# Performance work log

Hardware: AMD Instinct MI355X
Metric: run time of the kernel (lower is better)

Reference implementation:

```python
import jax, jax.numpy as jnp
import numpy as np

B, T, F = 2048, 256, 128
H = F  # hidden_size == feature_num in lstm0


def setup_inputs() -> dict:
    key = jax.random.key(0)
    ks = jax.random.split(key, 7)
    s = 1.0 / np.sqrt(H)  # torch LSTM/Linear default uniform init scale
    s_lin = 1.0 / np.sqrt(T * H)
    return {
        "x": jax.random.normal(ks[0], (B, T, F), dtype=jnp.float32),
        "w_ih": jax.random.uniform(ks[1], (4 * H, F), jnp.float32, -s, s),
        "w_hh": jax.random.uniform(ks[2], (4 * H, H), jnp.float32, -s, s),
        "b_ih": jax.random.uniform(ks[3], (4 * H,), jnp.float32, -s, s),
        "b_hh": jax.random.uniform(ks[4], (4 * H,), jnp.float32, -s, s),
        "w_lin": jax.random.uniform(ks[5], (1, T * H), jnp.float32, -s_lin, s_lin),
        "b_lin": jax.random.uniform(ks[6], (1,), jnp.float32, -s_lin, s_lin),
    }


def _lstm(x, w_ih, w_hh, b_ih, b_hh):
    # x: [B, T, F] -> h_seq: [B, T, H]; torch gate order: i, f, g, o
    b = x.shape[0]
    h_dim = w_hh.shape[1]
    # precompute input contribution for all timesteps: [B, T, 4H]
    xg = jnp.einsum('btf,gf->btg', x, w_ih) + b_ih + b_hh

    def step(carry, g_t):  # g_t: [B, 4H]
        h, c = carry
        gates = g_t + h @ w_hh.T
        i, f, g, o = jnp.split(gates, 4, axis=-1)
        c = jax.nn.sigmoid(f) * c + jax.nn.sigmoid(i) * jnp.tanh(g)
        h = jax.nn.sigmoid(o) * jnp.tanh(c)
        return (h, c), h

    init = (jnp.zeros((b, h_dim), x.dtype), jnp.zeros((b, h_dim), x.dtype))
    _, hs = jax.lax.scan(step, init, jnp.swapaxes(xg, 0, 1))  # hs: [T, B, H]
    return jnp.swapaxes(hs, 0, 1)


def reference(x, w_ih, w_hh, b_ih, b_hh, w_lin, b_lin):
    h = _lstm(x, w_ih, w_hh, b_ih, b_hh)          # [B, T, H]
    # Dropout(0.6) in eval mode == identity
    flat = h.reshape(h.shape[0], -1)               # [B, T*H]
    out = flat @ w_lin.T + b_lin                   # [B, 1]
    return out.reshape(-1)                          # [B]
```

## Files before the change

kernel.cpp:

```cpp
#include <hip/hip_runtime.h>


typedef __attribute__((ext_vector_type(8))) short short8;
typedef __attribute__((ext_vector_type(4))) float f32x4;
typedef __attribute__((ext_vector_type(2))) float f32x2;

#define T_STEPS 256
#define L2E 1.4426950408889634f

__device__ __forceinline__ unsigned int cvt_pk_bf16(float lo, float hi) {
    unsigned int r;
    asm volatile("v_cvt_pk_bf16_f32 %0, %1, %2" : "=v"(r) : "v"(lo), "v"(hi));
    return r;
}
__device__ __forceinline__ unsigned short f2bf(float f) {
    unsigned int u = __builtin_bit_cast(unsigned int, f);
    u += 0x7fffu + ((u >> 16) & 1u);
    return (unsigned short)(u >> 16);
}
__device__ __forceinline__ float rcp_fast(float x) { return __builtin_amdgcn_rcpf(x); }
__device__ __forceinline__ float exp2f_fast(float x) { return __builtin_amdgcn_exp2f(x); }

__device__ __forceinline__ short8 pack8(const f32x4 a, const f32x4 b) {
    short8 v;
    v[0] = (short)f2bf(a[0]); v[1] = (short)f2bf(a[1]);
    v[2] = (short)f2bf(a[2]); v[3] = (short)f2bf(a[3]);
    v[4] = (short)f2bf(b[0]); v[5] = (short)f2bf(b[1]);
    v[6] = (short)f2bf(b[2]); v[7] = (short)f2bf(b[3]);
    return v;
}

#define LBAR() asm volatile("s_waitcnt lgkmcnt(0)\n\ts_barrier" ::: "memory")

#define MFMA16(A, B, C) __builtin_amdgcn_mfma_f32_16x16x32_bf16((A), (B), (C), 0, 0, 0)

#define GATE(R, CS, WL, AJ, HO)                                                \
  { float gi = ch0[0][R] + ch1[0][R];                                          \
    float gf = ch0[1][R] + ch1[1][R];                                          \
    float gg = ch0[2][R] + ch1[2][R];                                          \
    float go = ch0[3][R] + ch1[3][R];                                          \
    float ef = exp2f_fast(gf * L2E);                                           \
    float ei = exp2f_fast(gi * L2E);                                           \
    float eg = exp2f_fast(gg * (2.f * L2E));                                   \
    float Fq = ef + 1.f, Iq = ei + 1.f, Gq = eg + 1.f;                         \
    float pq = Iq * Gq;                                                        \
    float Rq = rcp_fast(Fq * pq);                                              \
    float cq = __builtin_fmaf(ef * pq, (CS), (ei * Fq) * (eg - 1.f)) * Rq;     \
    (CS) = cq;                                                                 \
    float ccq = fminf(fmaxf(cq, -15.f), 15.f);                                 \
    float eo = exp2f_fast(go * L2E);                                           \
    float ec = exp2f_fast(ccq * (2.f * L2E));                                  \
    float oh = (eo * (ec - 1.f)) * rcp_fast((eo + 1.f) * (ec + 1.f));          \
    (AJ) = __builtin_fmaf(oh, (WL), (AJ));                                     \
    (HO) = oh; }

#define GROUP(T0, GP, GXC, GXN)                                                \
  do {                                                                         \
    const f32x4 zero4 = {0.f, 0.f, 0.f, 0.f};                                  \
    short8 afh[4], afx0, afx1;                                                 \
    f32x4 ch0[4], ch1[4];                                                      \
                         \
    _Pragma("unroll")                                                          \
    for (int kt = 0; kt < 4; ++kt)                                             \
      afh[kt] = *reinterpret_cast<const short8*>(&hbuf[0][hridx[kt]]);         \
    __builtin_amdgcn_s_setprio(1);                                             \
    _Pragma("unroll")                                                          \
    for (int n = 0; n < 4; ++n) ch0[n] = MFMA16(afh[0], bq[4][n], GXC[n]);     \
    _Pragma("unroll")                                                          \
    for (int n = 0; n < 4; ++n) ch1[n] = MFMA16(afh[2], bq[6][n], zero4);      \
    _Pragma("unroll")                                                          \
    for (int n = 0; n < 4; ++n) ch0[n] = MFMA16(afh[1], bq[5][n], ch0[n]);     \
    _Pragma("unroll")                                                          \
    for (int n = 0; n < 4; ++n) ch1[n] = MFMA16(afh[3], bq[7][n], ch1[n]);     \
    __builtin_amdgcn_s_setprio(0);                                             \
          \
    afx0 = *reinterpret_cast<const short8*>(&xbuf[GP][xridx[0]]);              \
    afx1 = *reinterpret_cast<const short8*>(&xbuf[GP][xridx[1]]);              \
    _Pragma("unroll")                                                          \
    for (int n = 0; n < 4; ++n)                                                \
      GXN[n] = (f32x4){bias[n], bias[n], bias[n], bias[n]};                    \
    _Pragma("unroll")                                                          \
    for (int n = 0; n < 4; ++n) GXN[n] = MFMA16(afx0, bq[0][n], GXN[n]);       \
    _Pragma("unroll")                                                          \
    for (int n = 0; n < 4; ++n) GXN[n] = MFMA16(afx1, bq[1][n], GXN[n]);       \
    {                      \
      const int tt = ((T0) + 4 < T_STEPS) ? (T0) + 4 : 0;                      \
      nx0 = *reinterpret_cast<const f32x2*>(xrow + (size_t)tt * 128);          \
      nx1 = *reinterpret_cast<const f32x2*>(xrow + (size_t)(tt + 1) * 128);    \
      const int tw = ((T0) + 2 < T_STEPS) ? (T0) + 2 : 0;                      \
      wlN0 = w_lin[tw * 128 + hid];                                            \
      wlN1 = w_lin[(tw + 1) * 128 + hid];                                      \
    }                                                                          \
    { float h0, h1;                                                            \
      GATE(0, cst0, wlA, acc0, h0);                                            \
      GATE(2, cst1, wlA, acc1, h1);                                            \
      unsigned int hpk = cvt_pk_bf16(h0, h1);                                  \
      hbuf[1][hwidx0] = (unsigned short)hpk;                                   \
      hbuf[1][hwidx1] = (unsigned short)(hpk >> 16); }                         \
    LBAR();                                                                    \
                         \
    _Pragma("unroll")                                                          \
    for (int kt = 0; kt < 4; ++kt)                                             \
      afh[kt] = *reinterpret_cast<const short8*>(&hbuf[1][hridx[kt]]);         \
    __builtin_amdgcn_s_setprio(1);                                             \
    _Pragma("unroll")                                                          \
    for (int n = 0; n < 4; ++n) ch0[n] = MFMA16(afh[0], bq[4][n], GXC[n]);     \
    _Pragma("unroll")                                                          \
    for (int n = 0; n < 4; ++n) ch1[n] = MFMA16(afh[2], bq[6][n], zero4);      \
    _Pragma("unroll")                                                          \
    for (int n = 0; n < 4; ++n) ch0[n] = MFMA16(afh[1], bq[5][n], ch0[n]);     \
    _Pragma("unroll")                                                          \
    for (int n = 0; n < 4; ++n) ch1[n] = MFMA16(afh[3], bq[7][n], ch1[n]);     \
    __builtin_amdgcn_s_setprio(0);                                             \
                                      \
    afx0 = *reinterpret_cast<const short8*>(&xbuf[GP][xridx[2]]);              \
    afx1 = *reinterpret_cast<const short8*>(&xbuf[GP][xridx[3]]);              \
    _Pragma("unroll")                                                          \
    for (int n = 0; n < 4; ++n) GXN[n] = MFMA16(afx0, bq[2][n], GXN[n]);       \
    _Pragma("unroll")                                                          \
    for (int n = 0; n < 4; ++n) GXN[n] = MFMA16(afx1, bq[3][n], GXN[n]);       \
    {                                   \
      *reinterpret_cast<unsigned int*>(&xbuf[(GP) ^ 1][xw0]) =                 \
          cvt_pk_bf16(nx0[0], nx0[1]);                                         \
      *reinterpret_cast<unsigned int*>(&xbuf[(GP) ^ 1][xw1]) =                 \
          cvt_pk_bf16(nx1[0], nx1[1]); }                                       \
    { float h0, h1;                                                            \
      GATE(1, cst0, wlB, acc0, h0);                                            \
      GATE(3, cst1, wlB, acc1, h1);                                            \
      unsigned int hpk = cvt_pk_bf16(h0, h1);                                  \
      hbuf[0][hwidx0] = (unsigned short)hpk;                                   \
      hbuf[0][hwidx1] = (unsigned short)(hpk >> 16); }                         \
    wlA = wlN0; wlB = wlN1;                                                    \
    LBAR();                                                                    \
  } while (0)

__global__ __launch_bounds__(512, 2) void lstm_fused_kernel(
    const float* __restrict__ x,
    const float* __restrict__ w_ih,
    const float* __restrict__ w_hh,
    const float* __restrict__ b_ih,
    const float* __restrict__ b_hh,
    const float* __restrict__ w_lin,
    const float* __restrict__ b_lin,
    float* __restrict__ out)
{
    __shared__ __align__(16) unsigned short xbuf[2][16 * 128];
    __shared__ __align__(16) unsigned short hbuf[2][8 * 128];
    __shared__ float redout[8][8];

    const int tid  = threadIdx.x;
    const int wave = tid >> 6;
    const int lane = tid & 63;
    const int c16  = lane & 15;
    const int kq   = lane >> 4;
    const int row0 = blockIdx.x * 8;
    const int hid  = wave * 16 + c16;

    reinterpret_cast<unsigned long long*>(hbuf)[tid] = 0ull;

    short8 bq[8][4];
#pragma unroll
    for (int kt = 0; kt < 8; ++kt) {
#pragma unroll
        for (int n = 0; n < 4; ++n) {
            const int G  = n * 128 + wave * 16 + c16;
            const int k0 = kt * 32 + kq * 8;
            const float* src = (kt < 4) ? (w_ih + G * 128 + k0)
                                        : (w_hh + G * 128 + (k0 - 128));
            f32x4 lo = *reinterpret_cast<const f32x4*>(src);
            f32x4 hi = *reinterpret_cast<const f32x4*>(src + 4);
            bq[kt][n] = pack8(lo, hi);
        }
    }
    float bias[4];
#pragma unroll
    for (int n = 0; n < 4; ++n) {
        const int G = n * 128 + wave * 16 + c16;
        bias[n] = b_ih[G] + b_hh[G];
    }

    int xridx[4], hridx[4];
    const int hcr = c16 >> 1;
#pragma unroll
    for (int kt = 0; kt < 4; ++kt) {
        xridx[kt] = (c16 * 128 + kt * 32 + kq * 8) ^ ((c16 & 7) << 3);
        hridx[kt] = hcr * 128 + ((kt * 32 + kq * 8) ^ (hcr << 3));
    }

    const int xr0 = wave * 2, xr1 = wave * 2 + 1;
    const int xw0 = (xr0 * 128 + lane * 2) ^ ((xr0 & 7) << 3);
    const int xw1 = (xr1 * 128 + lane * 2) ^ ((xr1 & 7) << 3);
    const float* xrow = x + (size_t)(row0 + wave) * T_STEPS * 128 + lane * 2;

    const int hwidx0 = ((2 * kq + 0) * 128 + hid) ^ ((2 * kq + 0) << 3);
    const int hwidx1 = ((2 * kq + 1) * 128 + hid) ^ ((2 * kq + 1) << 3);

    {
        f32x2 v0 = *reinterpret_cast<const f32x2*>(xrow);
        f32x2 v1 = *reinterpret_cast<const f32x2*>(xrow + 128);
        *reinterpret_cast<unsigned int*>(&xbuf[1][xw0]) = cvt_pk_bf16(v0[0], v0[1]);
        *reinterpret_cast<unsigned int*>(&xbuf[1][xw1]) = cvt_pk_bf16(v1[0], v1[1]);
    }
    __syncthreads();

    f32x4 gA[4], gB[4];
    {
        short8 afx[4];
#pragma unroll
        for (int kt = 0; kt < 4; ++kt)
            afx[kt] = *reinterpret_cast<const short8*>(&xbuf[1][xridx[kt]]);
#pragma unroll
        for (int n = 0; n < 4; ++n)
            gA[n] = (f32x4){bias[n], bias[n], bias[n], bias[n]};
#pragma unroll
        for (int kt = 0; kt < 4; ++kt)
#pragma unroll
            for (int n = 0; n < 4; ++n)
                gA[n] = MFMA16(afx[kt], bq[kt][n], gA[n]);
    }
    {
        f32x2 v2 = *reinterpret_cast<const f32x2*>(xrow + 2 * 128);
        f32x2 v3 = *reinterpret_cast<const f32x2*>(xrow + 3 * 128);
        *reinterpret_cast<unsigned int*>(&xbuf[0][xw0]) = cvt_pk_bf16(v2[0], v2[1]);
        *reinterpret_cast<unsigned int*>(&xbuf[0][xw1]) = cvt_pk_bf16(v3[0], v3[1]);
    }

    float cst0 = 0.f, cst1 = 0.f;
    float acc0 = 0.f, acc1 = 0.f;
    float wlA = w_lin[hid];
    float wlB = w_lin[128 + hid];
    float wlN0 = 0.f, wlN1 = 0.f;
    f32x2 nx0 = {0.f, 0.f}, nx1 = {0.f, 0.f};

    __syncthreads();

    for (int t = 0; t < T_STEPS; t += 4) {
        GROUP(t,     0, gA, gB);
        GROUP(t + 2, 1, gB, gA);
    }

#pragma unroll
    for (int r = 0; r < 2; ++r) {
        float v = (r == 0) ? acc0 : acc1;
        v += __shfl_xor(v, 1);
        v += __shfl_xor(v, 2);
        v += __shfl_xor(v, 4);
        v += __shfl_xor(v, 8);
        if (c16 == 0) redout[wave][2 * kq + r] = v;
    }
    __syncthreads();
    if (tid < 8) {
        float s = b_lin[0];
#pragma unroll
        for (int w = 0; w < 8; ++w) s += redout[w][tid];
        out[row0 + tid] = s;
    }
}

extern "C" void kernel_launch(void* const* d_in, const int* in_sizes, int n_in,
                              void* d_out, int out_size, void* d_ws, size_t ws_size,
                              hipStream_t stream) {
    const float* x     = (const float*)d_in[0];
    const float* w_ih  = (const float*)d_in[1];
    const float* w_hh  = (const float*)d_in[2];
    const float* b_ih  = (const float*)d_in[3];
    const float* b_hh  = (const float*)d_in[4];
    const float* w_lin = (const float*)d_in[5];
    const float* b_lin = (const float*)d_in[6];
    float* out = (float*)d_out;

    lstm_fused_kernel<<<256, 512, 0, stream>>>(x, w_ih, w_hh, b_ih, b_hh, w_lin, b_lin, out);
}
```

Before: 199.6 us.

## Split LSTM block into producer waves for input projection and consumer waves for recurrence

Doubles the block to 1024 threads. Waves 0-7 compute the x·W_ih projection for upcoming timesteps and stage the results in a new fp32 LDS buffer. Waves 8-15 do only the h·W_hh MFMAs plus the gate math, reading the staged projections. This takes the input-projection MFMAs off the serial recurrent critical path and halves the per-wave weight registers. In exchange it adds LDS traffic for the gate pre-activations, extra LDS footprint, and block-wide barriers shared across 16 waves, which can lower occupancy.

```diff
diff --git a/kernel.cpp b/kernel.cpp
--- a/kernel.cpp
+++ b/kernel.cpp
@@ -35,10 +35,10 @@
 #define MFMA16(A, B, C) __builtin_amdgcn_mfma_f32_16x16x32_bf16((A), (B), (C), 0, 0, 0)
 
 #define GATE(R, CS, WL, AJ, HO)                                                \
-  { float gi = ch0[0][R] + ch1[0][R];                                          \
-    float gf = ch0[1][R] + ch1[1][R];                                          \
-    float gg = ch0[2][R] + ch1[2][R];                                          \
-    float go = ch0[3][R] + ch1[3][R];                                          \
+  { float gi = ch_[0][R];                                                      \
+    float gf = ch_[1][R];                                                      \
+    float gg = ch_[2][R];                                                      \
+    float go = ch_[3][R];                                                      \
     float ef = exp2f_fast(gf * L2E);                                           \
     float ei = exp2f_fast(gi * L2E);                                           \
     float eg = exp2f_fast(gg * (2.f * L2E));                                   \
@@ -54,87 +54,69 @@
     (AJ) = __builtin_fmaf(oh, (WL), (AJ));                                     \
     (HO) = oh; }
 
-#define GROUP(T0, GP, GXC, GXN)                                                \
-  do {                                                                         \
-    const f32x4 zero4 = {0.f, 0.f, 0.f, 0.f};                                  \
-    short8 afh[4], afx0, afx1;                                                 \
-    f32x4 ch0[4], ch1[4];                                                      \
-                         \
+#define HSTEP(RP, WP, P, S, WLS)                                               \
+  { short8 af_[4];                                                             \
+    f32x4 ch_[4];                                                              \
     _Pragma("unroll")                                                          \
     for (int kt = 0; kt < 4; ++kt)                                             \
-      afh[kt] = *reinterpret_cast<const short8*>(&hbuf[0][hridx[kt]]);         \
-    __builtin_amdgcn_s_setprio(1);                                             \
-    _Pragma("unroll")                                                          \
-    for (int n = 0; n < 4; ++n) ch0[n] = MFMA16(afh[0], bq[4][n], GXC[n]);     \
-    _Pragma("unroll")                                                          \
-    for (int n = 0; n < 4; ++n) ch1[n] = MFMA16(afh[2], bq[6][n], zero4);      \
-    _Pragma("unroll")                                                          \
-    for (int n = 0; n < 4; ++n) ch0[n] = MFMA16(afh[1], bq[5][n], ch0[n]);     \
-    _Pragma("unroll")                                                          \
-    for (int n = 0; n < 4; ++n) ch1[n] = MFMA16(afh[3], bq[7][n], ch1[n]);     \
-    __builtin_amdgcn_s_setprio(0);                                             \
-          \
-    afx0 = *reinterpret_cast<const short8*>(&xbuf[GP][xridx[0]]);              \
-    afx1 = *reinterpret_cast<const short8*>(&xbuf[GP][xridx[1]]);              \
+      af_[kt] = *reinterpret_cast<const short8*>(&hbuf[RP][hridx[kt]]);        \
     _Pragma("unroll")                                                          \
     for (int n = 0; n < 4; ++n)                                                \
-      GXN[n] = (f32x4){bias[n], bias[n], bias[n], bias[n]};                    \
+      ch_[n] = *reinterpret_cast<const f32x4*>(&gXbuf[P][n][w8][goff]);        \
     _Pragma("unroll")                                                          \
-    for (int n = 0; n < 4; ++n) GXN[n] = MFMA16(afx0, bq[0][n], GXN[n]);       \
-    _Pragma("unroll")                                                          \
-    for (int n = 0; n < 4; ++n) GXN[n] = MFMA16(afx1, bq[1][n], GXN[n]);       \
-    {                      \
+    for (int kt = 0; kt < 4; ++kt)                                             \
+      _Pragma("unroll")                                                        \
+      for (int n = 0; n < 4; ++n)                                              \
+        ch_[n] = MFMA16(af_[kt], bq[kt][n], ch_[n]);                           \
+    float h0_, h1_;                                                            \
+    GATE((S), cst0, (WLS), acc0, h0_);                                         \
+    GATE((2 + (S)), cst1, (WLS), acc1, h1_);                                   \
+    unsigned int hpk_ = cvt_pk_bf16(h0_, h1_);                                 \
+    hbuf[WP][hwidx0] = (unsigned short)hpk_;                                   \
+    hbuf[WP][hwidx1] = (unsigned short)(hpk_ >> 16); }
+
+#define GROUPP(T0, P)                                                          \
+  {                                                  \
+    if (xw) {                             \
+      short8 af_[4];                                                           \
+      _Pragma("unroll")                                                        \
+      for (int kt = 0; kt < 4; ++kt)                                           \
+        af_[kt] = *reinterpret_cast<const short8*>(&xbuf[(P) ^ 1][xridx[kt]]); \
+      _Pragma("unroll")                                                        \
+      for (int n = 0; n < 4; ++n)                                              \
+        gx[n] = (f32x4){bias[n], bias[n], bias[n], bias[n]};                   \
+      _Pragma("unroll")                                                        \
+      for (int kt = 0; kt < 4; ++kt)                                           \
+        _Pragma("unroll")                                                      \
+        for (int n = 0; n < 4; ++n)                                            \
+          gx[n] = MFMA16(af_[kt], bq[kt][n], gx[n]);                           \
       const int tt = ((T0) + 4 < T_STEPS) ? (T0) + 4 : 0;                      \
       nx0 = *reinterpret_cast<const f32x2*>(xrow + (size_t)tt * 128);          \
       nx1 = *reinterpret_cast<const f32x2*>(xrow + (size_t)(tt + 1) * 128);    \
+    } else {                                                                   \
+      HSTEP(0, 1, (P), 0, wlA);                                                \
       const int tw = ((T0) + 2 < T_STEPS) ? (T0) + 2 : 0;                      \
       wlN0 = w_lin[tw * 128 + hid];                                            \
       wlN1 = w_lin[(tw + 1) * 128 + hid];                                      \
     }                                                                          \
-    { float h0, h1;                                                            \
-      GATE(0, cst0, wlA, acc0, h0);                                            \
-      GATE(2, cst1, wlA, acc1, h1);                                            \
-      unsigned int hpk = cvt_pk_bf16(h0, h1);                                  \
-      hbuf[1][hwidx0] = (unsigned short)hpk;                                   \
-      hbuf[1][hwidx1] = (unsigned short)(hpk >> 16); }                         \
     LBAR();                                                                    \
-                         \
-    _Pragma("unroll")                                                          \
-    for (int kt = 0; kt < 4; ++kt)                                             \
-      afh[kt] = *reinterpret_cast<const short8*>(&hbuf[1][hridx[kt]]);         \
-    __builtin_amdgcn_s_setprio(1);                                             \
-    _Pragma("unroll")                                                          \
-    for (int n = 0; n < 4; ++n) ch0[n] = MFMA16(afh[0], bq[4][n], GXC[n]);     \
-    _Pragma("unroll")                                                          \
-    for (int n = 0; n < 4; ++n) ch1[n] = MFMA16(afh[2], bq[6][n], zero4);      \
-    _Pragma("unroll")                                                          \
-    for (int n = 0; n < 4; ++n) ch0[n] = MFMA16(afh[1], bq[5][n], ch0[n]);     \
-    _Pragma("unroll")                                                          \
-    for (int n = 0; n < 4; ++n) ch1[n] = MFMA16(afh[3], bq[7][n], ch1[n]);     \
-    __builtin_amdgcn_s_setprio(0);                                             \
-                                      \
-    afx0 = *reinterpret_cast<const short8*>(&xbuf[GP][xridx[2]]);              \
-    afx1 = *reinterpret_cast<const short8*>(&xbuf[GP][xridx[3]]);              \
-    _Pragma("unroll")                                                          \
-    for (int n = 0; n < 4; ++n) GXN[n] = MFMA16(afx0, bq[2][n], GXN[n]);       \
-    _Pragma("unroll")                                                          \
-    for (int n = 0; n < 4; ++n) GXN[n] = MFMA16(afx1, bq[3][n], GXN[n]);       \
-    {                                   \
-      *reinterpret_cast<unsigned int*>(&xbuf[(GP) ^ 1][xw0]) =                 \
+                                                     \
+    if (xw) {                      \
+      _Pragma("unroll")                                                        \
+      for (int n = 0; n < 4; ++n)                                              \
+        *reinterpret_cast<f32x4*>(&gXbuf[(P) ^ 1][n][w8][goff]) = gx[n];       \
+      *reinterpret_cast<unsigned int*>(&xbuf[P][xw0]) =                        \
           cvt_pk_bf16(nx0[0], nx0[1]);                                         \
-      *reinterpret_cast<unsigned int*>(&xbuf[(GP) ^ 1][xw1]) =                 \
-          cvt_pk_bf16(nx1[0], nx1[1]); }                                       \
-    { float h0, h1;                                                            \
-      GATE(1, cst0, wlB, acc0, h0);                                            \
-      GATE(3, cst1, wlB, acc1, h1);                                            \
-      unsigned int hpk = cvt_pk_bf16(h0, h1);                                  \
-      hbuf[0][hwidx0] = (unsigned short)hpk;                                   \
-      hbuf[0][hwidx1] = (unsigned short)(hpk >> 16); }                         \
-    wlA = wlN0; wlB = wlN1;                                                    \
+      *reinterpret_cast<unsigned int*>(&xbuf[P][xw1]) =                        \
+          cvt_pk_bf16(nx1[0], nx1[1]);                                         \
+    } else {                                                                   \
+      HSTEP(1, 0, (P), 1, wlB);                                                \
+      wlA = wlN0; wlB = wlN1;                                                  \
+    }                                                                          \
     LBAR();                                                                    \
-  } while (0)
-
-__global__ __launch_bounds__(512, 2) void lstm_fused_kernel(
+  }
+
+__global__ __launch_bounds__(1024, 4) void lstm_fused_kernel(
     const float* __restrict__ x,
     const float* __restrict__ w_ih,
     const float* __restrict__ w_hh,
@@ -146,6 +128,7 @@
 {
     __shared__ __align__(16) unsigned short xbuf[2][16 * 128];
     __shared__ __align__(16) unsigned short hbuf[2][8 * 128];
+    __shared__ __align__(16) float gXbuf[2][4][8][256];
     __shared__ float redout[8][8];
 
     const int tid  = threadIdx.x;
@@ -154,29 +137,30 @@
     const int c16  = lane & 15;
     const int kq   = lane >> 4;
     const int row0 = blockIdx.x * 8;
-    const int hid  = wave * 16 + c16;
-
-    reinterpret_cast<unsigned long long*>(hbuf)[tid] = 0ull;
-
-    short8 bq[8][4];
-#pragma unroll
-    for (int kt = 0; kt < 8; ++kt) {
+    const bool xw  = (wave < 8);
+    const int w8   = wave & 7;
+    const int hid  = w8 * 16 + c16;
+
+    short8 bq[4][4];
+#pragma unroll
+    for (int kt = 0; kt < 4; ++kt) {
 #pragma unroll
         for (int n = 0; n < 4; ++n) {
-            const int G  = n * 128 + wave * 16 + c16;
+            const int G  = n * 128 + w8 * 16 + c16;
             const int k0 = kt * 32 + kq * 8;
-            const float* src = (kt < 4) ? (w_ih + G * 128 + k0)
-                                        : (w_hh + G * 128 + (k0 - 128));
+            const float* src = (xw ? w_ih : w_hh) + G * 128 + k0;
             f32x4 lo = *reinterpret_cast<const f32x4*>(src);
             f32x4 hi = *reinterpret_cast<const f32x4*>(src + 4);
             bq[kt][n] = pack8(lo, hi);
         }
     }
-    float bias[4];
-#pragma unroll
-    for (int n = 0; n < 4; ++n) {
-        const int G = n * 128 + wave * 16 + c16;
-        bias[n] = b_ih[G] + b_hh[G];
+    float bias[4] = {0.f, 0.f, 0.f, 0.f};
+    if (xw) {
+#pragma unroll
+        for (int n = 0; n < 4; ++n) {
+            const int G = n * 128 + w8 * 16 + c16;
+            bias[n] = b_ih[G] + b_hh[G];
+        }
     }
 
     int xridx[4], hridx[4];
@@ -186,67 +170,72 @@
         xridx[kt] = (c16 * 128 + kt * 32 + kq * 8) ^ ((c16 & 7) << 3);
         hridx[kt] = hcr * 128 + ((kt * 32 + kq * 8) ^ (hcr << 3));
     }
-
-    const int xr0 = wave * 2, xr1 = wave * 2 + 1;
+    const int goff = c16 * 16 + ((4 * kq) ^ (((c16 >> 1) & 3) << 2));
+
+    const int xr0 = w8 * 2, xr1 = w8 * 2 + 1;
     const int xw0 = (xr0 * 128 + lane * 2) ^ ((xr0 & 7) << 3);
     const int xw1 = (xr1 * 128 + lane * 2) ^ ((xr1 & 7) << 3);
-    const float* xrow = x + (size_t)(row0 + wave) * T_STEPS * 128 + lane * 2;
+    const float* xrow = x + (size_t)(row0 + w8) * T_STEPS * 128 + lane * 2;
 
     const int hwidx0 = ((2 * kq + 0) * 128 + hid) ^ ((2 * kq + 0) << 3);
     const int hwidx1 = ((2 * kq + 1) * 128 + hid) ^ ((2 * kq + 1) << 3);
 
-    {
+    if (xw) {
         f32x2 v0 = *reinterpret_cast<const f32x2*>(xrow);
         f32x2 v1 = *reinterpret_cast<const f32x2*>(xrow + 128);
-        *reinterpret_cast<unsigned int*>(&xbuf[1][xw0]) = cvt_pk_bf16(v0[0], v0[1]);
-        *reinterpret_cast<unsigned int*>(&xbuf[1][xw1]) = cvt_pk_bf16(v1[0], v1[1]);
-    }
-    __syncthreads();
-
-    f32x4 gA[4], gB[4];
-    {
-        short8 afx[4];
-#pragma unroll
-        for (int kt = 0; kt < 4; ++kt)
-            afx[kt] = *reinterpret_cast<const short8*>(&xbuf[1][xridx[kt]]);
-#pragma unroll
-        for (int n = 0; n < 4; ++n)
-            gA[n] = (f32x4){bias[n], bias[n], bias[n], bias[n]};
-#pragma unroll
-        for (int kt = 0; kt < 4; ++kt)
-#pragma unroll
-            for (int n = 0; n < 4; ++n)
-                gA[n] = MFMA16(afx[kt], bq[kt][n], gA[n]);
-    }
-    {
         f32x2 v2 = *reinterpret_cast<const f32x2*>(xrow + 2 * 128);
         f32x2 v3 = *reinterpret_cast<const f32x2*>(xrow + 3 * 128);
-        *reinterpret_cast<unsigned int*>(&xbuf[0][xw0]) = cvt_pk_bf16(v2[0], v2[1]);
-        *reinterpret_cast<unsigned int*>(&xbuf[0][xw1]) = cvt_pk_bf16(v3[0], v3[1]);
+        *reinterpret_cast<unsigned int*>(&xbuf[0][xw0]) = cvt_pk_bf16(v0[0], v0[1]);
+        *reinterpret_cast<unsigned int*>(&xbuf[0][xw1]) = cvt_pk_bf16(v1[0], v1[1]);
+        *reinterpret_cast<unsigned int*>(&xbuf[1][xw0]) = cvt_pk_bf16(v2[0], v2[1]);
+        *reinterpret_cast<unsigned int*>(&xbuf[1][xw1]) = cvt_pk_bf16(v3[0], v3[1]);
+    } else {
+        reinterpret_cast<unsigned long long*>(hbuf)[tid - 512] = 0ull;
+    }
+    __syncthreads();
+
+    f32x4 gx[4];
+    if (xw) {
+        short8 af_[4];
+#pragma unroll
+        for (int kt = 0; kt < 4; ++kt)
+            af_[kt] = *reinterpret_cast<const short8*>(&xbuf[0][xridx[kt]]);
+#pragma unroll
+        for (int n = 0; n < 4; ++n)
+            gx[n] = (f32x4){bias[n], bias[n], bias[n], bias[n]};
+#pragma unroll
+        for (int kt = 0; kt < 4; ++kt)
+#pragma unroll
+            for (int n = 0; n < 4; ++n)
+                gx[n] = MFMA16(af_[kt], bq[kt][n], gx[n]);
+#pragma unroll
+        for (int n = 0; n < 4; ++n)
+            *reinterpret_cast<f32x4*>(&gXbuf[0][n][w8][goff]) = gx[n];
     }
 
     float cst0 = 0.f, cst1 = 0.f;
     float acc0 = 0.f, acc1 = 0.f;
-    float wlA = w_lin[hid];
-    float wlB = w_lin[128 + hid];
-    float wlN0 = 0.f, wlN1 = 0.f;
+    float wlA = 0.f, wlB = 0.f, wlN0 = 0.f, wlN1 = 0.f;
+    if (!xw) { wlA = w_lin[hid]; wlB = w_lin[128 + hid]; }
     f32x2 nx0 = {0.f, 0.f}, nx1 = {0.f, 0.f};
 
     __syncthreads();
 
     for (int t = 0; t < T_STEPS; t += 4) {
-        GROUP(t,     0, gA, gB);
-        GROUP(t + 2, 1, gB, gA);
-    }
-
-#pragma unroll
-    for (int r = 0; r < 2; ++r) {
-        float v = (r == 0) ? acc0 : acc1;
-        v += __shfl_xor(v, 1);
-        v += __shfl_xor(v, 2);
-        v += __shfl_xor(v, 4);
-        v += __shfl_xor(v, 8);
-        if (c16 == 0) redout[wave][2 * kq + r] = v;
+        GROUPP(t, 0);
+        GROUPP(t + 2, 1);
+    }
+
+    if (!xw) {
+#pragma unroll
+        for (int r = 0; r < 2; ++r) {
+            float v = (r == 0) ? acc0 : acc1;
+            v += __shfl_xor(v, 1);
+            v += __shfl_xor(v, 2);
+            v += __shfl_xor(v, 4);
+            v += __shfl_xor(v, 8);
+            if (c16 == 0) redout[w8][2 * kq + r] = v;
+        }
     }
     __syncthreads();
     if (tid < 8) {
@@ -269,5 +258,5 @@
     const float* b_lin = (const float*)d_in[6];
     float* out = (float*)d_out;
 
-    lstm_fused_kernel<<<256, 512, 0, stream>>>(x, w_ih, w_hh, b_ih, b_hh, w_lin, b_lin, out);
-}
+    lstm_fused_kernel<<<256, 1024, 0, stream>>>(x, w_ih, w_hh, b_ih, b_hh, w_lin, b_lin, out);
+}
```

Measured after the change: 350.2 us. 1.75x slower.
